# Kernel tuning notes

Hardware: AMD Instinct MI355X
Metric: run time of the kernel (lower is better)

The kernel has to match this reference:

```python
import jax, jax.numpy as jnp
import numpy as np
from jax import lax

BN_EPS = 1e-5
BNS = 1.0 / np.sqrt(1.0 + BN_EPS)  # eval-mode BatchNorm with mean=0, var=1, gamma=1, beta=0


def setup_inputs() -> dict:
    key = jax.random.key(0)
    ks = jax.random.split(key, 12)
    B, Cin, H, W = 8, 256, 128, 128
    NC, HD, RC, NL = 12, 64, 128, 3
    f = lambda k, shp, s: jax.random.normal(k, shp, jnp.float32) * s
    return dict(
        features=f(ks[0], (B, Cin, H, W), 1.0),
        segmentation=jax.random.uniform(ks[1], (B, NC, H, W), dtype=jnp.float32),
        W_rpn=f(ks[2], (RC, Cin, 3, 3), 0.02), b_rpn=jnp.zeros((RC,), jnp.float32),
        W_node=f(ks[3], (HD, RC), 0.08), b_node=jnp.zeros((HD,), jnp.float32),
        W_e1=f(ks[4], (2 * HD, HD), 0.08), b_e1=jnp.zeros((HD,), jnp.float32),
        W_e2=f(ks[5], (HD, HD), 0.1), b_e2=jnp.zeros((HD,), jnp.float32),
        W_g=f(ks[6], (NL, HD, HD), 0.1), b_g=jnp.zeros((NL, HD), jnp.float32),
        ln_g=jnp.ones((NL, HD), jnp.float32), ln_b=jnp.zeros((NL, HD), jnp.float32),
        glob_emb=f(ks[7], (NC, HD), 0.02),
        W_sp=f(ks[8], (HD, RC), 0.1), b_sp=jnp.zeros((RC,), jnp.float32),
    )


def _forward(features, segmentation, W_rpn, b_rpn, W_node, b_node, W_e1, b_e1,
             W_e2, b_e2, W_g, b_g, ln_g, ln_b, glob_emb, W_sp, b_sp):
    B, NC, H, W = segmentation.shape
    HD = W_node.shape[0]
    NL = W_g.shape[0]

    # ---- RegionProposalNetwork: 3x3 conv + BN(eval) + ReLU ----
    refined = lax.conv_general_dilated(
        features, W_rpn, (1, 1), 'SAME',
        dimension_numbers=('NCHW', 'OIHW', 'NCHW'))
    refined = jax.nn.relu((refined + b_rpn[None, :, None, None]) * BNS)  # [B,RC,H,W]

    # per-class 3x3 maxpool on segmentation, threshold -> binary masks
    pooled = lax.reduce_window(segmentation, -jnp.inf, lax.max,
                               (1, 1, 3, 3), (1, 1, 1, 1), 'SAME')
    masks = (pooled > 0.5).astype(features.dtype)  # [B,NC,H,W]

    # ---- NodeFeatureExtractor (1x1 conv is linear: conv(f*m)=(Wf)*m + b) ----
    yw = jnp.einsum('dk,bkhw->bdhw', W_node, refined)            # [B,HD,H,W]
    z = jax.nn.relu((yw + b_node[None, :, None, None]) * BNS)    # value inside mask region
    masked_sum = jnp.einsum('bdhw,bchw->bcd', z, masks)          # [B,NC,HD]
    mask_sum = masks.sum((2, 3))                                 # [B,NC]
    node_feats = masked_sum / (mask_sum[..., None] + 1e-6)       # [B,NC,HD]

    # ---- EdgeFeatureExtractor: all (i,j), i!=j, gated by class presence ----
    pairs = np.array([(i, j) for i in range(NC) for j in range(NC) if i != j])
    src = jnp.asarray(pairs[:, 0])  # [E]
    dst = jnp.asarray(pairs[:, 1])
    present = (mask_sum > 0).astype(features.dtype)              # [B,NC]
    valid = present[:, src] * present[:, dst]                    # [B,E]
    cat = jnp.concatenate([node_feats[:, src], node_feats[:, dst]], axis=-1)  # [B,E,2HD]
    h = jax.nn.relu(cat @ W_e1 + b_e1)
    edge_attr = (h @ W_e2 + b_e2) * valid[..., None]             # [B,E,HD]

    # ---- TissueGraphNetwork ----
    presence = (node_feats.sum(-1) != 0).astype(features.dtype)[..., None]  # [B,NC,1]
    seg_sum = jax.vmap(lambda m: jax.ops.segment_sum(m, dst, num_segments=NC))
    x = node_feats
    for l in range(NL):
        xw = x @ W_g[l]                                          # [B,NC,HD]
        msgs = xw[:, src] * edge_attr                            # [B,E,HD]
        agg = seg_sum(msgs) + b_g[l]
        xr = jax.nn.relu(agg)
        mu = xr.mean(-1, keepdims=True)
        var = ((xr - mu) ** 2).mean(-1, keepdims=True)
        normed = (xr - mu) / jnp.sqrt(var + 1e-5) * ln_g[l] + ln_b[l]
        x = normed + x if l > 0 else normed
    x = x * presence + glob_emb[None] * (1.0 - presence)         # [B,NC,HD]

    # ---- SpatialProjector ----
    spatial = jnp.einsum('bcd,bchw->bdhw', x, masks)             # [B,HD,H,W]
    out = jnp.einsum('do,bdhw->bohw', W_sp, spatial)             # [B,RC,H,W]
    out = jax.nn.relu((out + b_sp[None, :, None, None]) * BNS)
    return out


def reference(features, segmentation, W_rpn, b_rpn, W_node, b_node, W_e1, b_e1,
              W_e2, b_e2, W_g, b_g, ln_g, ln_b, glob_emb, W_sp, b_sp):
    return _forward(features, segmentation, W_rpn, b_rpn, W_node, b_node,
                    W_e1, b_e1, W_e2, b_e2, W_g, b_g, ln_g, ln_b,
                    glob_emb, W_sp, b_sp)
```

## Files before the change

### kernel.cpp

```cpp
#include <hip/hip_runtime.h>
#include <math.h>

#define BNS_F 0.9999950000374998f

typedef short short8 __attribute__((ext_vector_type(8)));
typedef float f32x4 __attribute__((ext_vector_type(4)));
typedef __attribute__((address_space(3))) void lds_void;
typedef const __attribute__((address_space(1))) void glb_void;

__device__ __forceinline__ unsigned short f2bf(float f) {
    unsigned u = __builtin_bit_cast(unsigned, f);
    unsigned r = (u + 0x7fffu + ((u >> 16) & 1u)) >> 16;
    return (unsigned short)r;
}
__device__ __forceinline__ float bf2f(unsigned short h) {
    unsigned u = ((unsigned)h) << 16;
    return __builtin_bit_cast(float, u);
}

__global__ __launch_bounds__(256) void prep_kernel(
    const float* __restrict__ feat, unsigned short* __restrict__ Fbt,
    const float* __restrict__ Wrpn, unsigned short* __restrict__ Wr,
    const float* __restrict__ seg, float* __restrict__ masks,
    float* __restrict__ mask_sum)
{
    int bid = blockIdx.x;
    int t = threadIdx.x;

    if (bid < 16384) {
        int pxc = bid & 63;
        int icg = (bid >> 6) & 31;
        int b   = bid >> 11;
        int px  = pxc * 256 + t;
        const float* src = feat + ((size_t)(b * 256 + icg * 8)) * 16384 + px;
        unsigned v[4];
        #pragma unroll
        for (int i = 0; i < 4; ++i) {
            unsigned lo = f2bf(src[(size_t)(2 * i)     * 16384]);
            unsigned hi = f2bf(src[(size_t)(2 * i + 1) * 16384]);
            v[i] = lo | (hi << 16);
        }
        uint4 o; o.x = v[0]; o.y = v[1]; o.z = v[2]; o.w = v[3];
        *(uint4*)(Fbt + (((size_t)(b * 32 + icg) * 16384) + px) * 8) = o;
    } else if (bid < 16512) {
        int oc = bid - 16384;
        const float* src = Wrpn + ((size_t)oc * 256 + t) * 9;
        #pragma unroll
        for (int tap = 0; tap < 9; ++tap)
            Wr[((size_t)tap * 128 + oc) * 256 + t] = f2bf(src[tap]);
    } else {
        int mb = bid - 16512;
        int h = (mb & 63) * 2 + (t >> 7);
        int c = (mb >> 6) % 12;
        int b = mb / (64 * 12);
        int px = t & 127;

        const float* s = seg + ((size_t)(b * 12 + c) * 128) * 128;
        float m = -INFINITY;
        #pragma unroll
        for (int dy = -1; dy <= 1; ++dy) {
            int y = h + dy;
            if (y < 0 || y > 127) continue;
            #pragma unroll
            for (int dx = -1; dx <= 1; ++dx) {
                int x = px + dx;
                if (x < 0 || x > 127) continue;
                m = fmaxf(m, s[y * 128 + x]);
            }
        }
        float v = (m > 0.5f) ? 1.0f : 0.0f;
        masks[((size_t)(b * 12 + c) * 128 + h) * 128 + px] = v;

        float cnt = v;
        #pragma unroll
        for (int off = 1; off < 64; off <<= 1) cnt += __shfl_xor(cnt, off, 64);
        if ((t & 63) == 0) atomicAdd(&mask_sum[b * 12 + c], cnt);
    }
}

#define SWZ(col) (((col) >> 1) & 3)
#define BUF_BYTES 24960
#define CHUNK_ELEMS (4u * 16384u * 8u)

__global__ __launch_bounds__(512, 6) void conv_node_kernel(
    const unsigned short* __restrict__ Fbt, const unsigned short* __restrict__ Wr,
    const float* __restrict__ brpn, const float* __restrict__ Wnode,
    const float* __restrict__ bnode, const float* __restrict__ masks,
    const float* __restrict__ zero16, float* __restrict__ ms_rep)
{
    __shared__ __align__(16) unsigned char lds[49920];

    int wg = blockIdx.x;
    int bid = (wg & 7) * 128 + (wg >> 3);
    int h = bid & 127, b = bid >> 7;

    int t = threadIdx.x;
    int lane = t & 63;
    int wv = __builtin_amdgcn_readfirstlane(t >> 6);
    int mg = wv >> 1;
    int ng = wv & 1;
    int kg = lane >> 4;
    int ln15 = lane & 15;

    f32x4 acc[2][4];
    #pragma unroll
    for (int i = 0; i < 2; ++i)
        #pragma unroll
        for (int j = 0; j < 4; ++j) acc[i][j] = (f32x4){0.f, 0.f, 0.f, 0.f};

    const unsigned short* zp = (const unsigned short*)zero16;

    const unsigned short* pp[4];
    #pragma unroll
    for (int r = 0; r < 4; ++r) {
        int c = (r < 3) ? (r * 512 + t) : (1536 + t);
        bool act = (r < 3) || (t < 24);
        int sp = c & 3, cr = c >> 2;
        int col = cr % 130, row = cr / 130;
        int sl = (sp - SWZ(col)) & 3;
        int y = h - 1 + row, x = col - 1;
        bool in = act && ((unsigned)y < 128u) && ((unsigned)x < 128u);
        pp[r] = in ? (Fbt + (((size_t)(b * 32 + sl) * 16384) + y * 128 + x) * 8)
                   : zp;
    }

    auto stage = [&](int bsel) {
        #pragma unroll
        for (int r = 0; r < 3; ++r) {
            unsigned ldsoff = (unsigned)bsel * BUF_BYTES
                            + (unsigned)(r * 512 + wv * 64) * 16;
            __builtin_amdgcn_global_load_lds((glb_void*)pp[r],
                (lds_void*)(lds + ldsoff), 16, 0, 0);
            pp[r] += (pp[r] == zp) ? 0u : CHUNK_ELEMS;
        }
        if (t < 24) {
            unsigned ldsoff = (unsigned)bsel * BUF_BYTES + 1536u * 16;
            __builtin_amdgcn_global_load_lds((glb_void*)pp[3],
                (lds_void*)(lds + ldsoff), 16, 0, 0);
        }
        pp[3] += (pp[3] == zp) ? 0u : CHUNK_ELEMS;
    };

    stage(0);
    __syncthreads();

    for (int s = 0; s < 8; ++s) {
        int ic0 = s * 32;
        const unsigned char* buf = lds + (s & 1) * BUF_BYTES;

        #pragma unroll
        for (int dy = 0; dy < 3; ++dy) {
            #pragma unroll
            for (int dxi = 0; dxi < 3; ++dxi) {
                int tap = dy * 3 + dxi;
                const unsigned short* wp =
                    Wr + ((size_t)(tap * 128 + mg * 32 + ln15) * 256 + ic0 + kg * 8);
                short8 a0 = *(const short8*)wp;
                short8 a1 = *(const short8*)(wp + (size_t)16 * 256);
                #pragma unroll
                for (int np = 0; np < 2; ++np) {
                    short8 b0, b1;
                    {
                        int col0 = ng * 64 + (np * 2) * 16 + ln15 + dxi;
                        unsigned off0 = (unsigned)((dy * 130 + col0) * 4
                                        + ((kg + SWZ(col0)) & 3)) * 16;
                        b0 = *(const short8*)(buf + off0);
                        int col1 = col0 + 16;
                        unsigned off1 = (unsigned)((dy * 130 + col1) * 4
                                        + ((kg + SWZ(col1)) & 3)) * 16;
                        b1 = *(const short8*)(buf + off1);
                    }
                    acc[0][np * 2]     = __builtin_amdgcn_mfma_f32_16x16x32_bf16(
                        a0, b0, acc[0][np * 2], 0, 0, 0);
                    acc[1][np * 2]     = __builtin_amdgcn_mfma_f32_16x16x32_bf16(
                        a1, b0, acc[1][np * 2], 0, 0, 0);
                    acc[0][np * 2 + 1] = __builtin_amdgcn_mfma_f32_16x16x32_bf16(
                        a0, b1, acc[0][np * 2 + 1], 0, 0, 0);
                    acc[1][np * 2 + 1] = __builtin_amdgcn_mfma_f32_16x16x32_bf16(
                        a1, b1, acc[1][np * 2 + 1], 0, 0, 0);
                }
            }
        }

        if (s < 7) stage((s + 1) & 1);
        __syncthreads();
    }

    unsigned short* refined = (unsigned short*)lds;
    #pragma unroll
    for (int mt = 0; mt < 2; ++mt) {
        #pragma unroll
        for (int nt = 0; nt < 4; ++nt) {
            int px = ng * 64 + nt * 16 + ln15;
            #pragma unroll
            for (int r = 0; r < 4; ++r) {
                int oc = mg * 32 + mt * 16 + kg * 4 + r;
                float v = fmaxf((acc[mt][nt][r] + brpn[oc]) * BNS_F, 0.f);
                refined[oc * 130 + px] = f2bf(v);
            }
        }
    }
    __syncthreads();

    float z0[8], z1[8];
    #pragma unroll
    for (int j = 0; j < 8; ++j) { z0[j] = 0.f; z1[j] = 0.f; }
    const float* wn = Wnode + (size_t)wv * 8 * 128;
    for (int k = 0; k < 128; ++k) {
        float r0 = bf2f(refined[k * 130 + lane]);
        float r1 = bf2f(refined[k * 130 + 64 + lane]);
        #pragma unroll
        for (int j = 0; j < 8; ++j) {
            float w = wn[j * 128 + k];
            z0[j] = fmaf(w, r0, z0[j]);
            z1[j] = fmaf(w, r1, z1[j]);
        }
    }
    #pragma unroll
    for (int j = 0; j < 8; ++j) {
        float bb = bnode[wv * 8 + j];
        z0[j] = fmaxf((z0[j] + bb) * BNS_F, 0.f);
        z1[j] = fmaxf((z1[j] + bb) * BNS_F, 0.f);
    }

    int rep = bid & 7;
    const float* mrow = masks + ((size_t)b * 12 * 128 + h) * 128;
    float* msb = ms_rep + ((size_t)(rep * 8 + b) * 12) * 64 + wv * 8;
    for (int c = 0; c < 12; ++c) {
        float m0 = mrow[(size_t)c * 16384 + lane];
        float m1 = mrow[(size_t)c * 16384 + 64 + lane];
        #pragma unroll
        for (int j = 0; j < 8; ++j) {
            float v = fmaf(z0[j], m0, z1[j] * m1);
            #pragma unroll
            for (int off2 = 1; off2 < 64; off2 <<= 1) v += __shfl_xor(v, off2, 64);
            if (lane == 0) atomicAdd(&msb[c * 64 + j], v);
        }
    }
}

__global__ __launch_bounds__(256) void edge_kernel(
    const float* __restrict__ ms_rep, const float* __restrict__ mask_sum,
    const float* __restrict__ We1, const float* __restrict__ be1,
    const float* __restrict__ We2, const float* __restrict__ be2,
    float* __restrict__ ea_g)
{
    int gb = blockIdx.x;
    int b = gb / 33, eg = gb % 33;
    int wv = threadIdx.x >> 6, d = threadIdx.x & 63;
    int e = eg * 4 + wv;
    int src = e / 11, jj = e % 11;
    int dst = jj + (jj >= src ? 1 : 0);

    float mssrc = 0.f, msdst = 0.f;
    #pragma unroll
    for (int rep = 0; rep < 8; ++rep) {
        mssrc += ms_rep[((size_t)(rep * 8 + b) * 12 + src) * 64 + d];
        msdst += ms_rep[((size_t)(rep * 8 + b) * 12 + dst) * 64 + d];
    }
    float cs = mask_sum[b * 12 + src], cd = mask_sum[b * 12 + dst];
    float nsrc = mssrc / (cs + 1e-6f);
    float ndst = msdst / (cd + 1e-6f);

    float hv = be1[d];
    for (int k = 0; k < 64; ++k) hv = fmaf(__shfl(nsrc, k, 64), We1[k * 64 + d], hv);
    for (int k = 0; k < 64; ++k) hv = fmaf(__shfl(ndst, k, 64), We1[(64 + k) * 64 + d], hv);
    hv = fmaxf(hv, 0.f);
    float av = be2[d];
    for (int k = 0; k < 64; ++k) av = fmaf(__shfl(hv, k, 64), We2[k * 64 + d], av);

    float valid = ((cs > 0.f) ? 1.f : 0.f) * ((cd > 0.f) ? 1.f : 0.f);
    ea_g[((size_t)b * 132 + e) * 64 + d] = av * valid;
}

__global__ __launch_bounds__(256) void graph_kernel(
    const float* __restrict__ ms_rep, const float* __restrict__ mask_sum,
    const float* __restrict__ ea_g,
    const float* __restrict__ Wg, const float* __restrict__ bg,
    const float* __restrict__ lng, const float* __restrict__ lnb,
    const float* __restrict__ glob, const float* __restrict__ Wsp,
    float* __restrict__ xs_out)
{
    __shared__ float nf[12 * 64];
    __shared__ float x [12 * 64];
    __shared__ float xw[12 * 64];
    __shared__ float ea[132 * 64];
    __shared__ float presence[12];

    int b = blockIdx.x;
    int t = threadIdx.x;

    for (int i = t; i < 768; i += 256) {
        int c = i >> 6, d = i & 63;
        float ms = 0.f;
        #pragma unroll
        for (int rep = 0; rep < 8; ++rep)
            ms += ms_rep[((size_t)(rep * 8 + b) * 12 + c) * 64 + d];
        nf[i] = ms / (mask_sum[b * 12 + c] + 1e-6f);
    }
    for (int i = t; i < 132 * 64; i += 256) ea[i] = ea_g[(size_t)b * 8448 + i];
    __syncthreads();

    for (int i = t; i < 768; i += 256) {
        int c = i >> 6;
        float v = nf[i];
        #pragma unroll
        for (int off = 1; off < 64; off <<= 1) v += __shfl_xor(v, off, 64);
        if ((i & 63) == 0) presence[c] = (v != 0.f) ? 1.f : 0.f;
        x[i] = nf[i];
    }
    __syncthreads();

    for (int l = 0; l < 3; ++l) {
        const float* wg = Wg + l * 4096;
        for (int i = t; i < 768; i += 256) {
            int c = i >> 6, d = i & 63;
            float v = 0.f;
            for (int k = 0; k < 64; ++k) v = fmaf(x[c * 64 + k], wg[k * 64 + d], v);
            xw[i] = v;
        }
        __syncthreads();
        for (int i = t; i < 768; i += 256) {
            int j = i >> 6, d = i & 63;
            float agg = bg[l * 64 + d];
            #pragma unroll
            for (int src2 = 0; src2 < 12; ++src2) {
                if (src2 == j) continue;
                int jj2 = j - (j > src2 ? 1 : 0);
                int e = src2 * 11 + jj2;
                agg = fmaf(xw[src2 * 64 + d], ea[e * 64 + d], agg);
            }
            float xr = fmaxf(agg, 0.f);
            float s = xr;
            #pragma unroll
            for (int off = 1; off < 64; off <<= 1) s += __shfl_xor(s, off, 64);
            float mu = s * (1.f / 64.f);
            float df = xr - mu;
            float s2 = df * df;
            #pragma unroll
            for (int off = 1; off < 64; off <<= 1) s2 += __shfl_xor(s2, off, 64);
            float var = s2 * (1.f / 64.f);
            float normed = df * (1.0f / sqrtf(var + 1e-5f)) * lng[l * 64 + d]
                           + lnb[l * 64 + d];
            nf[i] = (l > 0) ? (normed + x[i]) : normed;
        }
        __syncthreads();
        for (int i = t; i < 768; i += 256) x[i] = nf[i];
        __syncthreads();
    }

    for (int i = t; i < 768; i += 256) {
        int c = i >> 6;
        float p = presence[c];
        x[i] = x[i] * p + glob[c * 64 + (i & 63)] * (1.f - p);
    }
    __syncthreads();

    for (int i = t; i < 12 * 128; i += 256) {
        int c = i >> 7, o = i & 127;
        float v = 0.f;
        for (int k = 0; k < 64; ++k) v = fmaf(x[c * 64 + k], Wsp[k * 128 + o], v);
        xs_out[b * 1536 + i] = v;
    }
}

__global__ __launch_bounds__(256) void out_kernel(
    const float* __restrict__ xs, const float* __restrict__ masks,
    const float* __restrict__ bsp, float* __restrict__ out)
{
    __shared__ float xsl[12 * 128];
    __shared__ float ml[12 * 128];
    int bid = blockIdx.x;
    int h = bid & 127;
    int b = bid >> 7;
    int t = threadIdx.x;

    for (int i = t; i < 1536; i += 256) xsl[i] = xs[b * 1536 + i];
    for (int i = t; i < 1536; i += 256) {
        int c = i >> 7, px = i & 127;
        ml[i] = masks[((size_t)(b * 12 + c) * 128 + h) * 128 + px];
    }
    __syncthreads();

    int px = t & 127;
    int og = t >> 7;
    float m[12];
    #pragma unroll
    for (int c = 0; c < 12; ++c) m[c] = ml[c * 128 + px];

    float* ob = out + ((size_t)b * 128 * 128 + h) * 128 + px;
    for (int i = 0; i < 64; ++i) {
        int o = og * 64 + i;
        float s = 0.f;
        #pragma unroll
        for (int c = 0; c < 12; ++c) s = fmaf(xsl[c * 128 + o], m[c], s);
        ob[(size_t)o * 16384] = fmaxf((s + bsp[o]) * BNS_F, 0.f);
    }
}

extern "C" void kernel_launch(void* const* d_in, const int* in_sizes, int n_in,
                              void* d_out, int out_size, void* d_ws, size_t ws_size,
                              hipStream_t stream)
{
    const float* feat  = (const float*)d_in[0];
    const float* seg   = (const float*)d_in[1];
    const float* Wrpn  = (const float*)d_in[2];
    const float* brpn  = (const float*)d_in[3];
    const float* Wnode = (const float*)d_in[4];
    const float* bnode = (const float*)d_in[5];
    const float* We1   = (const float*)d_in[6];
    const float* be1   = (const float*)d_in[7];
    const float* We2   = (const float*)d_in[8];
    const float* be2   = (const float*)d_in[9];
    const float* Wg    = (const float*)d_in[10];
    const float* bg    = (const float*)d_in[11];
    const float* lng   = (const float*)d_in[12];
    const float* lnb   = (const float*)d_in[13];
    const float* glob  = (const float*)d_in[14];
    const float* Wsp   = (const float*)d_in[15];
    const float* bsp   = (const float*)d_in[16];
    float* out = (float*)d_out;

    unsigned short* Fbt = (unsigned short*)d_out;

    float* masks    = (float*)d_ws;
    float* ms_rep   = masks + 1572864;
    float* mask_sum = ms_rep + 49152;
    float* zero16   = mask_sum + 96;
    float* xs       = zero16 + 8;
    float* ea_g     = xs + 12288;
    unsigned short* Wr = (unsigned short*)(ea_g + 67584);

    hipMemsetAsync(ms_rep, 0, (49152 + 96 + 8) * sizeof(float), stream);

    prep_kernel<<<22656, 256, 0, stream>>>(feat, Fbt, Wrpn, Wr, seg, masks, mask_sum);
    conv_node_kernel<<<1024, 512, 0, stream>>>(Fbt, Wr, brpn, Wnode, bnode,
                                               masks, zero16, ms_rep);
    edge_kernel<<<264, 256, 0, stream>>>(ms_rep, mask_sum, We1, be1, We2, be2, ea_g);
    graph_kernel<<<8, 256, 0, stream>>>(ms_rep, mask_sum, ea_g,
                                        Wg, bg, lng, lnb, glob, Wsp, xs);
    out_kernel<<<1024, 256, 0, stream>>>(xs, masks, bsp, out);
}
```

Before: 492.5 us.

## Replace LDS-staged conv tiles with direct global B-fragment loads, 256-thread blocks

The conv kernel no longer double-buffers input halo tiles into LDS through global_load_lds. Each wave now loads its B fragments straight from global memory, using clamped coordinates and zero-masking for padding. Blocks shrink to 256 threads, each wave covers 64 output channels by 32 pixels, and a row is processed in two 64-pixel halves so the LDS buffer for the refined tile is much smaller. This removes LDS staging and barriers from the K loop, but it relies on cache for the 3x reuse across taps, doubles the A-fragment loads per output, and adds more atomics per block.

```diff
diff --git a/kernel.cpp b/kernel.cpp
--- a/kernel.cpp
+++ b/kernel.cpp
@@ -5,8 +5,6 @@
 
 typedef short short8 __attribute__((ext_vector_type(8)));
 typedef float f32x4 __attribute__((ext_vector_type(4)));
-typedef __attribute__((address_space(3))) void lds_void;
-typedef const __attribute__((address_space(1))) void glb_void;
 
 __device__ __forceinline__ unsigned short f2bf(float f) {
     unsigned u = __builtin_bit_cast(unsigned, f);
@@ -78,17 +76,15 @@
     }
 }
 
-#define SWZ(col) (((col) >> 1) & 3)
-#define BUF_BYTES 24960
-#define CHUNK_ELEMS (4u * 16384u * 8u)
-
-__global__ __launch_bounds__(512, 6) void conv_node_kernel(
+#define CHUNK_STEP (4u * 16384u * 8u)
+
+__global__ __launch_bounds__(256, 4) void conv_node_kernel(
     const unsigned short* __restrict__ Fbt, const unsigned short* __restrict__ Wr,
     const float* __restrict__ brpn, const float* __restrict__ Wnode,
     const float* __restrict__ bnode, const float* __restrict__ masks,
-    const float* __restrict__ zero16, float* __restrict__ ms_rep)
-{
-    __shared__ __align__(16) unsigned char lds[49920];
+    float* __restrict__ ms_rep)
+{
+    __shared__ unsigned short refined[128 * 66];
 
     int wg = blockIdx.x;
     int bid = (wg & 7) * 128 + (wg >> 3);
@@ -102,140 +98,114 @@
     int kg = lane >> 4;
     int ln15 = lane & 15;
 
-    f32x4 acc[2][4];
+    unsigned rowBase[3];
+    bool ybad[3];
     #pragma unroll
-    for (int i = 0; i < 2; ++i)
-        #pragma unroll
-        for (int j = 0; j < 4; ++j) acc[i][j] = (f32x4){0.f, 0.f, 0.f, 0.f};
-
-    const unsigned short* zp = (const unsigned short*)zero16;
-
-    const unsigned short* pp[4];
-    #pragma unroll
-    for (int r = 0; r < 4; ++r) {
-        int c = (r < 3) ? (r * 512 + t) : (1536 + t);
-        bool act = (r < 3) || (t < 24);
-        int sp = c & 3, cr = c >> 2;
-        int col = cr % 130, row = cr / 130;
-        int sl = (sp - SWZ(col)) & 3;
-        int y = h - 1 + row, x = col - 1;
-        bool in = act && ((unsigned)y < 128u) && ((unsigned)x < 128u);
-        pp[r] = in ? (Fbt + (((size_t)(b * 32 + sl) * 16384) + y * 128 + x) * 8)
-                   : zp;
-    }
-
-    auto stage = [&](int bsel) {
-        #pragma unroll
-        for (int r = 0; r < 3; ++r) {
-            unsigned ldsoff = (unsigned)bsel * BUF_BYTES
-                            + (unsigned)(r * 512 + wv * 64) * 16;
-            __builtin_amdgcn_global_load_lds((glb_void*)pp[r],
-                (lds_void*)(lds + ldsoff), 16, 0, 0);
-            pp[r] += (pp[r] == zp) ? 0u : CHUNK_ELEMS;
-        }
-        if (t < 24) {
-            unsigned ldsoff = (unsigned)bsel * BUF_BYTES + 1536u * 16;
-            __builtin_amdgcn_global_load_lds((glb_void*)pp[3],
-                (lds_void*)(lds + ldsoff), 16, 0, 0);
-        }
-        pp[3] += (pp[3] == zp) ? 0u : CHUNK_ELEMS;
-    };
-
-    stage(0);
-    __syncthreads();
-
-    for (int s = 0; s < 8; ++s) {
-        int ic0 = s * 32;
-        const unsigned char* buf = lds + (s & 1) * BUF_BYTES;
-
-        #pragma unroll
-        for (int dy = 0; dy < 3; ++dy) {
+    for (int dy = 0; dy < 3; ++dy) {
+        int y = h - 1 + dy;
+        int yc = y < 0 ? 0 : (y > 127 ? 127 : y);
+        ybad[dy] = (y != yc);
+        rowBase[dy] = ((unsigned)(b * 32 + kg) * 16384u + (unsigned)yc * 128u) * 8u;
+    }
+
+    int rep = bid & 7;
+    float* msb = ms_rep + ((size_t)(rep * 8 + b) * 12) * 64 + wv * 16;
+    const float* mrow = masks + ((size_t)b * 12 * 128 + h) * 128;
+
+    for (int half = 0; half < 2; ++half) {
+        unsigned xo[6];
+        bool xbad[6];
+        #pragma unroll
+        for (int nt = 0; nt < 2; ++nt)
             #pragma unroll
             for (int dxi = 0; dxi < 3; ++dxi) {
-                int tap = dy * 3 + dxi;
-                const unsigned short* wp =
-                    Wr + ((size_t)(tap * 128 + mg * 32 + ln15) * 256 + ic0 + kg * 8);
-                short8 a0 = *(const short8*)wp;
-                short8 a1 = *(const short8*)(wp + (size_t)16 * 256);
+                int xr = half * 64 + ng * 32 + nt * 16 + ln15 + dxi - 1;
+                int xc = xr < 0 ? 0 : (xr > 127 ? 127 : xr);
+                xbad[nt * 3 + dxi] = (xr != xc);
+                xo[nt * 3 + dxi] = (unsigned)xc * 8u;
+            }
+
+        f32x4 acc[4][2];
+        #pragma unroll
+        for (int f = 0; f < 4; ++f)
+            #pragma unroll
+            for (int nt = 0; nt < 2; ++nt) acc[f][nt] = (f32x4){0.f, 0.f, 0.f, 0.f};
+
+        unsigned ri0 = rowBase[0], ri1 = rowBase[1], ri2 = rowBase[2];
+
+        for (int s = 0; s < 8; ++s) {
+            int ic0 = s * 32;
+            #pragma unroll
+            for (int dy = 0; dy < 3; ++dy) {
+                unsigned rb = (dy == 0) ? ri0 : ((dy == 1) ? ri1 : ri2);
+                bool yb = ybad[dy];
                 #pragma unroll
-                for (int np = 0; np < 2; ++np) {
-                    short8 b0, b1;
-                    {
-                        int col0 = ng * 64 + (np * 2) * 16 + ln15 + dxi;
-                        unsigned off0 = (unsigned)((dy * 130 + col0) * 4
-                                        + ((kg + SWZ(col0)) & 3)) * 16;
-                        b0 = *(const short8*)(buf + off0);
-                        int col1 = col0 + 16;
-                        unsigned off1 = (unsigned)((dy * 130 + col1) * 4
-                                        + ((kg + SWZ(col1)) & 3)) * 16;
-                        b1 = *(const short8*)(buf + off1);
-                    }
-                    acc[0][np * 2]     = __builtin_amdgcn_mfma_f32_16x16x32_bf16(
-                        a0, b0, acc[0][np * 2], 0, 0, 0);
-                    acc[1][np * 2]     = __builtin_amdgcn_mfma_f32_16x16x32_bf16(
-                        a1, b0, acc[1][np * 2], 0, 0, 0);
-                    acc[0][np * 2 + 1] = __builtin_amdgcn_mfma_f32_16x16x32_bf16(
-                        a0, b1, acc[0][np * 2 + 1], 0, 0, 0);
-                    acc[1][np * 2 + 1] = __builtin_amdgcn_mfma_f32_16x16x32_bf16(
-                        a1, b1, acc[1][np * 2 + 1], 0, 0, 0);
+                for (int dxi = 0; dxi < 3; ++dxi) {
+                    int tap = dy * 3 + dxi;
+                    const unsigned short* wp = Wr
+                        + ((size_t)(tap * 128 + mg * 64 + ln15) * 256 + ic0 + kg * 8);
+                    short8 a0 = *(const short8*)wp;
+                    short8 a1 = *(const short8*)(wp + 16 * 256);
+                    short8 a2 = *(const short8*)(wp + 32 * 256);
+                    short8 a3 = *(const short8*)(wp + 48 * 256);
+
+                    short8 b0 = *(const short8*)(Fbt + rb + xo[dxi]);
+                    short8 b1 = *(const short8*)(Fbt + rb + xo[3 + dxi]);
+                    if (yb | xbad[dxi])     b0 = (short8)0;
+                    if (yb | xbad[3 + dxi]) b1 = (short8)0;
+
+                    acc[0][0] = __builtin_amdgcn_mfma_f32_16x16x32_bf16(a0, b0, acc[0][0], 0, 0, 0);
+                    acc[1][0] = __builtin_amdgcn_mfma_f32_16x16x32_bf16(a1, b0, acc[1][0], 0, 0, 0);
+                    acc[2][0] = __builtin_amdgcn_mfma_f32_16x16x32_bf16(a2, b0, acc[2][0], 0, 0, 0);
+                    acc[3][0] = __builtin_amdgcn_mfma_f32_16x16x32_bf16(a3, b0, acc[3][0], 0, 0, 0);
+                    acc[0][1] = __builtin_amdgcn_mfma_f32_16x16x32_bf16(a0, b1, acc[0][1], 0, 0, 0);
+                    acc[1][1] = __builtin_amdgcn_mfma_f32_16x16x32_bf16(a1, b1, acc[1][1], 0, 0, 0);
+                    acc[2][1] = __builtin_amdgcn_mfma_f32_16x16x32_bf16(a2, b1, acc[2][1], 0, 0, 0);
+                    acc[3][1] = __builtin_amdgcn_mfma_f32_16x16x32_bf16(a3, b1, acc[3][1], 0, 0, 0);
                 }
             }
-        }
-
-        if (s < 7) stage((s + 1) & 1);
+            ri0 += CHUNK_STEP; ri1 += CHUNK_STEP; ri2 += CHUNK_STEP;
+        }
+
+        #pragma unroll
+        for (int f = 0; f < 4; ++f)
+            #pragma unroll
+            for (int nt = 0; nt < 2; ++nt)
+                #pragma unroll
+                for (int r = 0; r < 4; ++r) {
+                    int oc = mg * 64 + f * 16 + kg * 4 + r;
+                    int pxl = ng * 32 + nt * 16 + ln15;
+                    float v = fmaxf((acc[f][nt][r] + brpn[oc]) * BNS_F, 0.f);
+                    refined[oc * 66 + pxl] = f2bf(v);
+                }
         __syncthreads();
-    }
-
-    unsigned short* refined = (unsigned short*)lds;
-    #pragma unroll
-    for (int mt = 0; mt < 2; ++mt) {
-        #pragma unroll
-        for (int nt = 0; nt < 4; ++nt) {
-            int px = ng * 64 + nt * 16 + ln15;
-            #pragma unroll
-            for (int r = 0; r < 4; ++r) {
-                int oc = mg * 32 + mt * 16 + kg * 4 + r;
-                float v = fmaxf((acc[mt][nt][r] + brpn[oc]) * BNS_F, 0.f);
-                refined[oc * 130 + px] = f2bf(v);
+
+        float z[16];
+        #pragma unroll
+        for (int j = 0; j < 16; ++j) z[j] = 0.f;
+        const float* wn = Wnode + (size_t)wv * 16 * 128;
+        for (int k = 0; k < 128; ++k) {
+            float rv = bf2f(refined[k * 66 + lane]);
+            #pragma unroll
+            for (int j = 0; j < 16; ++j)
+                z[j] = fmaf(wn[j * 128 + k], rv, z[j]);
+        }
+        #pragma unroll
+        for (int j = 0; j < 16; ++j)
+            z[j] = fmaxf((z[j] + bnode[wv * 16 + j]) * BNS_F, 0.f);
+
+        #pragma unroll 2
+        for (int c = 0; c < 12; ++c) {
+            float m = mrow[(size_t)c * 16384 + half * 64 + lane];
+            #pragma unroll
+            for (int j = 0; j < 16; ++j) {
+                float v = z[j] * m;
+                #pragma unroll
+                for (int off = 1; off < 64; off <<= 1) v += __shfl_xor(v, off, 64);
+                if (lane == j) atomicAdd(&msb[c * 64 + j], v);
             }
         }
-    }
-    __syncthreads();
-
-    float z0[8], z1[8];
-    #pragma unroll
-    for (int j = 0; j < 8; ++j) { z0[j] = 0.f; z1[j] = 0.f; }
-    const float* wn = Wnode + (size_t)wv * 8 * 128;
-    for (int k = 0; k < 128; ++k) {
-        float r0 = bf2f(refined[k * 130 + lane]);
-        float r1 = bf2f(refined[k * 130 + 64 + lane]);
-        #pragma unroll
-        for (int j = 0; j < 8; ++j) {
-            float w = wn[j * 128 + k];
-            z0[j] = fmaf(w, r0, z0[j]);
-            z1[j] = fmaf(w, r1, z1[j]);
-        }
-    }
-    #pragma unroll
-    for (int j = 0; j < 8; ++j) {
-        float bb = bnode[wv * 8 + j];
-        z0[j] = fmaxf((z0[j] + bb) * BNS_F, 0.f);
-        z1[j] = fmaxf((z1[j] + bb) * BNS_F, 0.f);
-    }
-
-    int rep = bid & 7;
-    const float* mrow = masks + ((size_t)b * 12 * 128 + h) * 128;
-    float* msb = ms_rep + ((size_t)(rep * 8 + b) * 12) * 64 + wv * 8;
-    for (int c = 0; c < 12; ++c) {
-        float m0 = mrow[(size_t)c * 16384 + lane];
-        float m1 = mrow[(size_t)c * 16384 + 64 + lane];
-        #pragma unroll
-        for (int j = 0; j < 8; ++j) {
-            float v = fmaf(z0[j], m0, z1[j] * m1);
-            #pragma unroll
-            for (int off2 = 1; off2 < 64; off2 <<= 1) v += __shfl_xor(v, off2, 64);
-            if (lane == 0) atomicAdd(&msb[c * 64 + j], v);
-        }
+        __syncthreads();
     }
 }
 
@@ -426,16 +396,15 @@
     float* masks    = (float*)d_ws;
     float* ms_rep   = masks + 1572864;
     float* mask_sum = ms_rep + 49152;
-    float* zero16   = mask_sum + 96;
-    float* xs       = zero16 + 8;
+    float* xs       = mask_sum + 96;
     float* ea_g     = xs + 12288;
     unsigned short* Wr = (unsigned short*)(ea_g + 67584);
 
-    hipMemsetAsync(ms_rep, 0, (49152 + 96 + 8) * sizeof(float), stream);
+    hipMemsetAsync(ms_rep, 0, (49152 + 96) * sizeof(float), stream);
 
     prep_kernel<<<22656, 256, 0, stream>>>(feat, Fbt, Wrpn, Wr, seg, masks, mask_sum);
-    conv_node_kernel<<<1024, 512, 0, stream>>>(Fbt, Wr, brpn, Wnode, bnode,
-                                               masks, zero16, ms_rep);
+    conv_node_kernel<<<1024, 256, 0, stream>>>(Fbt, Wr, brpn, Wnode, bnode,
+                                               masks, ms_rep);
     edge_kernel<<<264, 256, 0, stream>>>(ms_rep, mask_sum, We1, be1, We2, be2, ea_g);
     graph_kernel<<<8, 256, 0, stream>>>(ms_rep, mask_sum, ea_g,
                                         Wg, bg, lng, lnb, glob, Wsp, xs);
```

Measured after the change: 618.8 us. 1.26x slower.

## Switch conv MFMA to 32x32x16 tiles with slot-major LDS layout

Applied to the files above, without the earlier changes.

Replaces the 16x16x32 bf16 MFMA tiling (2x4 tiles per wave) with 32x32x16 MFMA (two 32x32 accumulators per wave) and reassigns waves to a 2x4 grid of 64 channels by 32 pixels. The LDS staging layout moves from a swizzled interleaved layout to a row/slot/column layout, and the pointer increment is precomputed instead of compared against the zero pointer each stage. The occupancy hint in launch bounds is dropped. The aim is fewer LDS reads and instructions per MFMA; the risks are LDS bank conflicts without the swizzle and a change in register pressure and occupancy.

```diff
diff --git a/kernel.cpp b/kernel.cpp
--- a/kernel.cpp
+++ b/kernel.cpp
@@ -4,7 +4,8 @@
 #define BNS_F 0.9999950000374998f
 
 typedef short short8 __attribute__((ext_vector_type(8)));
-typedef float f32x4 __attribute__((ext_vector_type(4)));
+typedef float f32x16 __attribute__((ext_vector_type(16)));
+
 typedef __attribute__((address_space(3))) void lds_void;
 typedef const __attribute__((address_space(1))) void glb_void;
 
@@ -78,11 +79,10 @@
     }
 }
 
-#define SWZ(col) (((col) >> 1) & 3)
 #define BUF_BYTES 24960
-#define CHUNK_ELEMS (4u * 16384u * 8u)
-
-__global__ __launch_bounds__(512, 6) void conv_node_kernel(
+#define CHUNK_STEP (4u * 16384u * 8u)
+
+__global__ __launch_bounds__(512) void conv_node_kernel(
     const unsigned short* __restrict__ Fbt, const unsigned short* __restrict__ Wr,
     const float* __restrict__ brpn, const float* __restrict__ Wnode,
     const float* __restrict__ bnode, const float* __restrict__ masks,
@@ -97,31 +97,31 @@
     int t = threadIdx.x;
     int lane = t & 63;
     int wv = __builtin_amdgcn_readfirstlane(t >> 6);
-    int mg = wv >> 1;
-    int ng = wv & 1;
-    int kg = lane >> 4;
-    int ln15 = lane & 15;
-
-    f32x4 acc[2][4];
-    #pragma unroll
-    for (int i = 0; i < 2; ++i)
-        #pragma unroll
-        for (int j = 0; j < 4; ++j) acc[i][j] = (f32x4){0.f, 0.f, 0.f, 0.f};
+    int mw = wv >> 2;
+    int nw = wv & 3;
+    int ln31 = lane & 31;
+    int khalf = lane >> 5;
+    int px0 = nw * 32;
+
+    f32x16 acc0 = (f32x16)0.f, acc1 = (f32x16)0.f;
 
     const unsigned short* zp = (const unsigned short*)zero16;
 
     const unsigned short* pp[4];
+    unsigned inc[4];
     #pragma unroll
     for (int r = 0; r < 4; ++r) {
         int c = (r < 3) ? (r * 512 + t) : (1536 + t);
         bool act = (r < 3) || (t < 24);
-        int sp = c & 3, cr = c >> 2;
-        int col = cr % 130, row = cr / 130;
-        int sl = (sp - SWZ(col)) & 3;
+        int row = c / 520;
+        int rem = c - row * 520;
+        int slot = rem / 130;
+        int col = rem - slot * 130;
         int y = h - 1 + row, x = col - 1;
         bool in = act && ((unsigned)y < 128u) && ((unsigned)x < 128u);
-        pp[r] = in ? (Fbt + (((size_t)(b * 32 + sl) * 16384) + y * 128 + x) * 8)
+        pp[r] = in ? (Fbt + (((size_t)(b * 32 + slot) * 16384) + y * 128 + x) * 8)
                    : zp;
+        inc[r] = in ? CHUNK_STEP : 0u;
     }
 
     auto stage = [&](int bsel) {
@@ -131,14 +131,14 @@
                             + (unsigned)(r * 512 + wv * 64) * 16;
             __builtin_amdgcn_global_load_lds((glb_void*)pp[r],
                 (lds_void*)(lds + ldsoff), 16, 0, 0);
-            pp[r] += (pp[r] == zp) ? 0u : CHUNK_ELEMS;
+            pp[r] += inc[r];
         }
         if (t < 24) {
             unsigned ldsoff = (unsigned)bsel * BUF_BYTES + 1536u * 16;
             __builtin_amdgcn_global_load_lds((glb_void*)pp[3],
                 (lds_void*)(lds + ldsoff), 16, 0, 0);
         }
-        pp[3] += (pp[3] == zp) ? 0u : CHUNK_ELEMS;
+        pp[3] += inc[3];
     };
 
     stage(0);
@@ -149,35 +149,27 @@
         const unsigned char* buf = lds + (s & 1) * BUF_BYTES;
 
         #pragma unroll
-        for (int dy = 0; dy < 3; ++dy) {
-            #pragma unroll
-            for (int dxi = 0; dxi < 3; ++dxi) {
-                int tap = dy * 3 + dxi;
-                const unsigned short* wp =
-                    Wr + ((size_t)(tap * 128 + mg * 32 + ln15) * 256 + ic0 + kg * 8);
-                short8 a0 = *(const short8*)wp;
-                short8 a1 = *(const short8*)(wp + (size_t)16 * 256);
+        for (int ks = 0; ks < 2; ++ks) {
+            #pragma unroll
+            for (int dy = 0; dy < 3; ++dy) {
                 #pragma unroll
-                for (int np = 0; np < 2; ++np) {
-                    short8 b0, b1;
-                    {
-                        int col0 = ng * 64 + (np * 2) * 16 + ln15 + dxi;
-                        unsigned off0 = (unsigned)((dy * 130 + col0) * 4
-                                        + ((kg + SWZ(col0)) & 3)) * 16;
-                        b0 = *(const short8*)(buf + off0);
-                        int col1 = col0 + 16;
-                        unsigned off1 = (unsigned)((dy * 130 + col1) * 4
-                                        + ((kg + SWZ(col1)) & 3)) * 16;
-                        b1 = *(const short8*)(buf + off1);
-                    }
-                    acc[0][np * 2]     = __builtin_amdgcn_mfma_f32_16x16x32_bf16(
-                        a0, b0, acc[0][np * 2], 0, 0, 0);
-                    acc[1][np * 2]     = __builtin_amdgcn_mfma_f32_16x16x32_bf16(
-                        a1, b0, acc[1][np * 2], 0, 0, 0);
-                    acc[0][np * 2 + 1] = __builtin_amdgcn_mfma_f32_16x16x32_bf16(
-                        a0, b1, acc[0][np * 2 + 1], 0, 0, 0);
-                    acc[1][np * 2 + 1] = __builtin_amdgcn_mfma_f32_16x16x32_bf16(
-                        a1, b1, acc[1][np * 2 + 1], 0, 0, 0);
+                for (int dxi = 0; dxi < 3; ++dxi) {
+                    int tap = dy * 3 + dxi;
+                    const unsigned short* wp = Wr
+                        + ((size_t)(tap * 128 + mw * 64 + ln31) * 256
+                           + ic0 + ks * 16 + khalf * 8);
+                    short8 a0 = *(const short8*)wp;
+                    short8 a1 = *(const short8*)(wp + 32 * 256);
+
+                    unsigned off = (unsigned)dy * 8320u
+                                 + (unsigned)(2 * ks + khalf) * 2080u
+                                 + (unsigned)(px0 + ln31 + dxi) * 16u;
+                    short8 bf = *(const short8*)(buf + off);
+
+                    acc0 = __builtin_amdgcn_mfma_f32_32x32x16_bf16(
+                        a0, bf, acc0, 0, 0, 0);
+                    acc1 = __builtin_amdgcn_mfma_f32_32x32x16_bf16(
+                        a1, bf, acc1, 0, 0, 0);
                 }
             }
         }
@@ -187,18 +179,16 @@
     }
 
     unsigned short* refined = (unsigned short*)lds;
-    #pragma unroll
-    for (int mt = 0; mt < 2; ++mt) {
-        #pragma unroll
-        for (int nt = 0; nt < 4; ++nt) {
-            int px = ng * 64 + nt * 16 + ln15;
-            #pragma unroll
-            for (int r = 0; r < 4; ++r) {
-                int oc = mg * 32 + mt * 16 + kg * 4 + r;
-                float v = fmaxf((acc[mt][nt][r] + brpn[oc]) * BNS_F, 0.f);
-                refined[oc * 130 + px] = f2bf(v);
-            }
-        }
+    int px = px0 + ln31;
+    #pragma unroll
+    for (int reg = 0; reg < 16; ++reg) {
+        int row = (reg & 3) + 8 * (reg >> 2) + 4 * khalf;
+        int oc0 = mw * 64 + row;
+        float v0 = fmaxf((acc0[reg] + brpn[oc0]) * BNS_F, 0.f);
+        refined[oc0 * 130 + px] = f2bf(v0);
+        int oc1 = oc0 + 32;
+        float v1 = fmaxf((acc1[reg] + brpn[oc1]) * BNS_F, 0.f);
+        refined[oc1 * 130 + px] = f2bf(v1);
     }
     __syncthreads();
 
```

New measurement: 566.2 us. +15.0%, slower.
